# Optimization experiments

Hardware: AMD Instinct MI355X
Metric: run time of the kernel (lower is better)

## Reference

```python
import jax, jax.numpy as jnp
import numpy as np

NOT_EPSILON = 1.0
B, Q, K, T = 2, 512, 512, 256  # batch, num queries, num keys, dims


def swishmax(x, axis):
    # x * exp(x - max) / (sum(|x * exp(x - max)|) + 1)
    xexp = x * jnp.exp(x - jnp.max(x, axis=axis, keepdims=True))
    return xexp / (jnp.sum(jnp.abs(xexp), axis=axis, keepdims=True) + NOT_EPSILON)


def setup_inputs() -> dict:
    key = jax.random.key(0)
    ks = jax.random.split(key, 8)
    s = 1.0 / np.sqrt(T)
    return {
        "query_tokens": jax.random.normal(ks[0], (B, Q, T), jnp.float32),
        "key_tokens": jax.random.normal(ks[1], (B, K, T), jnp.float32),
        "value_tokens": jax.random.normal(ks[2], (B, K, T), jnp.float32),
        "Wk": jax.random.normal(ks[3], (T, T), jnp.float32) * s,
        "Wq": jax.random.normal(ks[4], (T, T), jnp.float32) * s,
        "Wva": jax.random.normal(ks[5], (T, T), jnp.float32) * s,
        "Wal": jax.random.normal(ks[6], (T, T), jnp.float32) * s,
        "Wvo": jax.random.normal(ks[7], (T, T), jnp.float32) * s,
    }


def reference(query_tokens, key_tokens, value_tokens, Wk, Wq, Wva, Wal, Wvo):
    # torch nn.Linear: y = x @ W.T (no biases)
    k = jnp.einsum('bkt,ut->bku', key_tokens, Wk)      # [B,K,T]
    q = jnp.einsum('bqt,ut->bqu', query_tokens, Wq)    # [B,Q,T]
    # elementwise outer product over token pairs: [B,K,Q,T]
    raw = k[:, :, None, :] * q[:, None, :, :]
    logits = jnp.einsum('bkqt,ut->bkqu', raw, Wal)     # [B,K,Q,T]
    scale = swishmax(logits, axis=-2)                  # normalize over Q
    v = jnp.einsum('bkt,ut->bku', value_tokens, Wva)   # [B,K,T]
    values_scaled = v[:, :, None, :] * scale           # [B,K,Q,T]
    value_sum = values_scaled.sum(axis=-3)             # sum over K -> [B,Q,T]
    return jnp.einsum('bqt,ut->bqu', value_sum, Wvo)   # [B,Q,T]
```

## Files before the change

### kernel.cpp

```cpp
#include <hip/hip_runtime.h>
#include <cstdint>


typedef short bf16x8 __attribute__((ext_vector_type(8)));
typedef float f32x4  __attribute__((ext_vector_type(4)));

__device__ inline float bf2f(short s) {
  return __uint_as_float(((unsigned)(unsigned short)s) << 16);
}
__device__ inline unsigned packrn(float lo, float hi) {
  return __builtin_amdgcn_perm(__float_as_uint(hi) + 0x8000u,
                               __float_as_uint(lo) + 0x8000u, 0x07060302u);
}
__device__ inline unsigned encM(float f) {
  unsigned k = (unsigned)__float_as_int(f);
  return (k & 0x80000000u) ? ~k : (k | 0x80000000u);
}
__device__ inline float decM(unsigned k) {
  int i = (k & 0x80000000u) ? (int)(k ^ 0x80000000u) : (int)~k;
  return __int_as_float(i);
}

#define FMA16()                                                                 \
  c[0][0] += a.x*w.x; c[0][1] += a.x*w.y; c[0][2] += a.x*w.z; c[0][3] += a.x*w.w; \
  c[1][0] += a.y*w.x; c[1][1] += a.y*w.y; c[1][2] += a.y*w.z; c[1][3] += a.y*w.w; \
  c[2][0] += a.z*w.x; c[2][1] += a.z*w.y; c[2][2] += a.z*w.z; c[2][3] += a.z*w.w; \
  c[3][0] += a.w*w.x; c[3][1] += a.w*w.y; c[3][2] += a.w*w.z; c[3][3] += a.w*w.w;

#define GEMM_BODY_RM(X, W)                                                      \
  __shared__ __align__(16) float As[16][68];                                    \
  __shared__ __align__(16) float Ws[16][68];                                    \
  const int tid = threadIdx.x;                                                  \
  const int tx4 = (tid & 15) * 4;                                               \
  const int ty4 = (tid >> 4) * 4;                                               \
  const int m0 = blockIdx.x * 64, u0 = blockIdx.y * 64;                         \
  const int lmi = tid >> 2, lc4 = (tid & 3) * 4;                                \
  float c[4][4] = {};                                                           \
  _Pragma("unroll 1")                                                           \
  for (int t0 = 0; t0 < 256; t0 += 16) {                                        \
    const float4 xa = *(const float4*)&(X)[(size_t)(m0 + lmi) * 256 + t0 + lc4];\
    const float4 wb = *(const float4*)&(W)[(size_t)(u0 + lmi) * 256 + t0 + lc4];\
    __syncthreads();                                                            \
    As[lc4 + 0][lmi] = xa.x; As[lc4 + 1][lmi] = xa.y;                           \
    As[lc4 + 2][lmi] = xa.z; As[lc4 + 3][lmi] = xa.w;                           \
    Ws[lc4 + 0][lmi] = wb.x; Ws[lc4 + 1][lmi] = wb.y;                           \
    Ws[lc4 + 2][lmi] = wb.z; Ws[lc4 + 3][lmi] = wb.w;                           \
    __syncthreads();                                                            \
    _Pragma("unroll")                                                           \
    for (int t = 0; t < 16; ++t) {                                              \
      const float4 a = *(const float4*)&As[t][ty4];                             \
      const float4 w = *(const float4*)&Ws[t][tx4];                             \
      FMA16();                                                                  \
    }                                                                           \
  }

__global__ __launch_bounds__(256) void proj3(
    const float* __restrict__ key, const float* __restrict__ value,
    const float* __restrict__ query, const float* __restrict__ Wk,
    const float* __restrict__ Wq, const float* __restrict__ Wva,
    const float* __restrict__ Wal, float* __restrict__ kproj,
    float* __restrict__ vproj, short* __restrict__ qpF,
    short* __restrict__ WalF, float* __restrict__ vsum)
{
  const int z = blockIdx.z;
  if (z == 3) {
    const int p = blockIdx.x * 4 + blockIdx.y;
    const int t256 = threadIdx.x;
#pragma unroll
    for (int e = 0; e < 4; ++e) {
      const int d = p * 1024 + t256 * 4 + e;
      const int j = d & 7, uu = (d >> 3) & 31, c8g = d >> 8;
      const int ucx = c8g >> 5, cc = c8g & 31;
      const float v = Wal[(ucx * 32 + uu) * 256 + cc * 8 + j];
      WalF[d] = (short)packrn(v, v);
    }
    float4* vz = (float4*)(vsum + p * 4096);
#pragma unroll
    for (int e = 0; e < 4; ++e) vz[t256 * 4 + e] = make_float4(0.f, 0.f, 0.f, 0.f);
    return;
  }
  const float* X = (z == 0) ? key : (z == 1) ? value : query;
  const float* W = (z == 0) ? Wk  : (z == 1) ? Wva   : Wq;
  GEMM_BODY_RM(X, W);
  if (z == 2) {
    const int tbase = u0 + tx4;
    const int ks = tbase >> 5, l4f = (tbase & 31) >> 3, j0 = tbase & 7;
#pragma unroll
    for (int i = 0; i < 4; ++i) {
      const int m = m0 + ty4 + i;
      const int bb = m >> 9, q = m & 511;
      const int g = q >> 4, l15q = q & 15;
      const size_t idx = ((size_t)(((bb * 32 + g) * 8 + ks) * 64) + l4f * 16 + l15q) * 8 + j0;
      uint2 s; s.x = packrn(c[i][0], c[i][1]); s.y = packrn(c[i][2], c[i][3]);
      *(uint2*)&qpF[idx] = s;
    }
  } else {
    float* C = (z == 0) ? kproj : vproj;
#pragma unroll
    for (int i = 0; i < 4; ++i)
      *(float4*)&C[(size_t)(m0 + ty4 + i) * 256 + u0 + tx4] =
          make_float4(c[i][0], c[i][1], c[i][2], c[i][3]);
  }
}

__global__ __launch_bounds__(256) void gemm_out(
    const float* __restrict__ X, const float* __restrict__ W, float* __restrict__ out)
{
  GEMM_BODY_RM(X, W);
#pragma unroll
  for (int i = 0; i < 4; ++i)
    *(float4*)&out[(size_t)(m0 + ty4 + i) * 256 + u0 + tx4] =
        make_float4(c[i][0], c[i][1], c[i][2], c[i][3]);
}

union Frag { bf16x8 v; unsigned u[4]; };

__global__ __launch_bounds__(512, 2) void kernelC(
    const short* __restrict__ qpF, const float* __restrict__ kproj,
    const float* __restrict__ vproj, const short* __restrict__ WalF,
    float* __restrict__ vsum)
{
  __shared__ __align__(16) short W2F[2][8192];
  __shared__ float vpS[32 * 33];
  __shared__ unsigned statM[96];
  __shared__ float statS[96];

  const int kt = blockIdx.x, uc = blockIdx.y, b = blockIdx.z;
  const int u0 = uc * 32, k0 = kt * 32;
  const int tid = threadIdx.x;
  const int lane = tid & 63, w = tid >> 6;
  const int l15 = lane & 15, l4 = lane >> 4;
  const int uu = tid & 31, c8 = tid >> 5;

  if (tid < 96) { statM[tid] = 0u; statS[tid] = 0.f; }
  {
    const int kk = tid >> 4, uu2 = (tid & 15) * 2;
    const float2 v2 = *(const float2*)&vproj[(size_t)(b * 512 + k0 + kk) * 256 + u0 + uu2];
    vpS[kk * 33 + uu2] = v2.x; vpS[kk * 33 + uu2 + 1] = v2.y;
  }

  float wl0[8], wl1[8];
  {
    const bf16x8 w0 = *(const bf16x8*)&WalF[((size_t)(uc * 32 + c8) * 32 + uu) * 8];
    const bf16x8 w1 = *(const bf16x8*)&WalF[((size_t)(uc * 32 + c8 + 16) * 32 + uu) * 8];
#pragma unroll
    for (int j = 0; j < 8; ++j) { wl0[j] = bf2f(w0[j]); wl1[j] = bf2f(w1[j]); }
  }

  const short* qbase = qpF + (size_t)b * 131072;
  Frag qa[4][8];
#pragma unroll
  for (int qg = 0; qg < 4; ++qg)
#pragma unroll
    for (int ks = 0; ks < 8; ++ks) {
      qa[qg][ks].v = *(const bf16x8*)&qbase[(((size_t)(w * 4 + qg) * 8 + ks) * 64 + lane) * 8];
      asm volatile("" : "+v"(qa[qg][ks].u[0]), "+v"(qa[qg][ks].u[1]),
                        "+v"(qa[qg][ks].u[2]), "+v"(qa[qg][ks].u[3]));
    }

  const int fb = (l4 * 32 + l15) * 8;
  const float* kq = &kproj[(long)(b * 512 + k0) * 256 + c8 * 8];

  {
    const f32x4 a0 = *(const f32x4*)(kq);
    const f32x4 a1 = *(const f32x4*)(kq + 4);
    const f32x4 b0 = *(const f32x4*)(kq + 128);
    const f32x4 b1 = *(const f32x4*)(kq + 132);
    uint4 st;
    st.x = packrn(wl0[0] * a0[0], wl0[1] * a0[1]);
    st.y = packrn(wl0[2] * a0[2], wl0[3] * a0[3]);
    st.z = packrn(wl0[4] * a1[0], wl0[5] * a1[1]);
    st.w = packrn(wl0[6] * a1[2], wl0[7] * a1[3]);
    *(uint4*)&W2F[0][(c8 * 32 + uu) * 8] = st;
    st.x = packrn(wl1[0] * b0[0], wl1[1] * b0[1]);
    st.y = packrn(wl1[2] * b0[2], wl1[3] * b0[3]);
    st.z = packrn(wl1[4] * b1[0], wl1[5] * b1[1]);
    st.w = packrn(wl1[6] * b1[2], wl1[7] * b1[3]);
    *(uint4*)&W2F[0][((c8 + 16) * 32 + uu) * 8] = st;
  }
  __syncthreads();

  const f32x4 z4 = {0.f, 0.f, 0.f, 0.f};
  f32x4 acc[4][2] = {z4, z4, z4, z4, z4, z4, z4, z4};

#pragma unroll 1
  for (int kk = 0; kk < 32; ++kk) {
    const int cs = kk & 1, ss = kk % 3;

    f32x4 a0, a1, b0, b1;
    if (kk < 31) {
      const float* kn = kq + (size_t)(kk + 1) * 256;
      a0 = *(const f32x4*)(kn);
      a1 = *(const f32x4*)(kn + 4);
      b0 = *(const f32x4*)(kn + 128);
      b1 = *(const f32x4*)(kn + 132);
    }

    f32x4 lg[4][2] = {z4, z4, z4, z4, z4, z4, z4, z4};
#pragma unroll
    for (int ks = 0; ks < 8; ++ks) {
      const bf16x8 f0 = *(const bf16x8*)&W2F[cs][fb + ks * 1024];
      const bf16x8 f1 = *(const bf16x8*)&W2F[cs][fb + ks * 1024 + 128];
#pragma unroll
      for (int qg = 0; qg < 4; ++qg) {
        lg[qg][0] = __builtin_amdgcn_mfma_f32_16x16x32_bf16(qa[qg][ks].v, f0, lg[qg][0], 0, 0, 0);
        lg[qg][1] = __builtin_amdgcn_mfma_f32_16x16x32_bf16(qa[qg][ks].v, f1, lg[qg][1], 0, 0, 0);
      }
    }
#pragma unroll
    for (int qg = 0; qg < 4; ++qg)
      asm volatile("" : "+v"(lg[qg][0]), "+v"(lg[qg][1]));

    if (kk < 31) {
      uint4 st;
      st.x = packrn(wl0[0] * a0[0], wl0[1] * a0[1]);
      st.y = packrn(wl0[2] * a0[2], wl0[3] * a0[3]);
      st.z = packrn(wl0[4] * a1[0], wl0[5] * a1[1]);
      st.w = packrn(wl0[6] * a1[2], wl0[7] * a1[3]);
      *(uint4*)&W2F[cs ^ 1][(c8 * 32 + uu) * 8] = st;
      st.x = packrn(wl1[0] * b0[0], wl1[1] * b0[1]);
      st.y = packrn(wl1[2] * b0[2], wl1[3] * b0[3]);
      st.z = packrn(wl1[4] * b1[0], wl1[5] * b1[1]);
      st.w = packrn(wl1[6] * b1[2], wl1[7] * b1[3]);
      *(uint4*)&W2F[cs ^ 1][((c8 + 16) * 32 + uu) * 8] = st;
    }

    float Mv[2], Sv[2];
#pragma unroll
    for (int ug = 0; ug < 2; ++ug) {
      const float m0q = fmaxf(fmaxf(lg[0][ug][0], lg[0][ug][1]), fmaxf(lg[0][ug][2], lg[0][ug][3]));
      const float m1q = fmaxf(fmaxf(lg[1][ug][0], lg[1][ug][1]), fmaxf(lg[1][ug][2], lg[1][ug][3]));
      const float m2q = fmaxf(fmaxf(lg[2][ug][0], lg[2][ug][1]), fmaxf(lg[2][ug][2], lg[2][ug][3]));
      const float m3q = fmaxf(fmaxf(lg[3][ug][0], lg[3][ug][1]), fmaxf(lg[3][ug][2], lg[3][ug][3]));
      float m = fmaxf(fmaxf(m0q, m1q), fmaxf(m2q, m3q));
      float sq[4];
#pragma unroll
      for (int qg = 0; qg < 4; ++qg) {
        float p0 = lg[qg][ug][0] * __expf(lg[qg][ug][0]);
        float p1 = lg[qg][ug][1] * __expf(lg[qg][ug][1]);
        float p2 = lg[qg][ug][2] * __expf(lg[qg][ug][2]);
        float p3 = lg[qg][ug][3] * __expf(lg[qg][ug][3]);
        lg[qg][ug][0] = p0; lg[qg][ug][1] = p1;
        lg[qg][ug][2] = p2; lg[qg][ug][3] = p3;
        sq[qg] = (fabsf(p0) + fabsf(p1)) + (fabsf(p2) + fabsf(p3));
      }
      float s = (sq[0] + sq[1]) + (sq[2] + sq[3]);
      m = fmaxf(m, __shfl_xor(m, 16));
      m = fmaxf(m, __shfl_xor(m, 32));
      s += __shfl_xor(s, 16);
      s += __shfl_xor(s, 32);
      Mv[ug] = m; Sv[ug] = s;
    }
    if (l4 == 0) {
      atomicMax(&statM[ss * 32 + l15],      encM(Mv[0]));
      atomicMax(&statM[ss * 32 + 16 + l15], encM(Mv[1]));
      atomicAdd(&statS[ss * 32 + l15],      Sv[0]);
      atomicAdd(&statS[ss * 32 + 16 + l15], Sv[1]);
    }
    __syncthreads();

#pragma unroll
    for (int ug = 0; ug < 2; ++ug) {
      const int ui = ug * 16 + l15;
      const float M = decM(statM[ss * 32 + ui]);
      const float S = statS[ss * 32 + ui];
      const float em = __expf(-M);
      const float g = vpS[kk * 33 + ui] * em * __builtin_amdgcn_rcpf(fmaf(S, em, 1.0f));
#pragma unroll
      for (int qg = 0; qg < 4; ++qg)
#pragma unroll
        for (int i = 0; i < 4; ++i)
          acc[qg][ug][i] = fmaf(g, lg[qg][ug][i], acc[qg][ug][i]);
    }
#pragma unroll
    for (int qg = 0; qg < 4; ++qg)
      asm volatile("" : "+v"(acc[qg][0]), "+v"(acc[qg][1]));

    const int rs = (kk + 2) % 3;
    if (tid < 32) { statM[rs * 32 + tid] = 0u; statS[rs * 32 + tid] = 0.f; }
  }

#pragma unroll
  for (int qg = 0; qg < 4; ++qg)
#pragma unroll
    for (int ug = 0; ug < 2; ++ug)
#pragma unroll
      for (int i = 0; i < 4; ++i)
        atomicAdd(&vsum[(size_t)(b * 512 + w * 64 + qg * 16 + l4 * 4 + i) * 256 +
                        u0 + ug * 16 + l15],
                  acc[qg][ug][i]);
}

extern "C" void kernel_launch(void* const* d_in, const int* in_sizes, int n_in,
                              void* d_out, int out_size, void* d_ws, size_t ws_size,
                              hipStream_t stream) {
  const float* query = (const float*)d_in[0];
  const float* key   = (const float*)d_in[1];
  const float* value = (const float*)d_in[2];
  const float* Wk    = (const float*)d_in[3];
  const float* Wq    = (const float*)d_in[4];
  const float* Wva   = (const float*)d_in[5];
  const float* Wal   = (const float*)d_in[6];
  const float* Wvo   = (const float*)d_in[7];
  float* ws = (float*)d_ws;

  float* kproj = ws;
  float* vproj = kproj + 262144;
  float* vsum  = vproj + 262144;
  short* qpF   = (short*)(vsum + 262144);
  short* WalF  = qpF + 262144;
  float* out   = (float*)d_out;

  proj3<<<dim3(16, 4, 4), 256, 0, stream>>>(key, value, query, Wk, Wq, Wva, Wal,
                                            kproj, vproj, qpF, WalF, vsum);
  kernelC<<<dim3(16, 8, 2), 512, 0, stream>>>(qpF, kproj, vproj, WalF, vsum);
  gemm_out<<<dim3(16, 4), 256, 0, stream>>>(vsum, Wvo, out);
}
```

Baseline: 192.3 us.

## Shrink GEMM tiles to 32 rows, prefetch next slab, split-K output GEMM

The shared FP32 GEMM body now uses 32x64 tiles instead of 64x64, which doubles the block count for the projection kernels and the output GEMM so more CUs are busy. The next K-slab is loaded from global memory while the current one is computed, a register prefetch. The output GEMM is split into two K halves that accumulate into the output with atomicAdd, so the proj3 kernel now also zeroes the output buffer. The costs are atomics and nondeterministic summation order, half of the A-loading threads idle, and extra zeroing work.

```diff
diff --git a/kernel.cpp b/kernel.cpp
--- a/kernel.cpp
+++ b/kernel.cpp
@@ -21,36 +21,39 @@
   return __int_as_float(i);
 }
 
-#define FMA16()                                                                 \
-  c[0][0] += a.x*w.x; c[0][1] += a.x*w.y; c[0][2] += a.x*w.z; c[0][3] += a.x*w.w; \
-  c[1][0] += a.y*w.x; c[1][1] += a.y*w.y; c[1][2] += a.y*w.z; c[1][3] += a.y*w.w; \
-  c[2][0] += a.z*w.x; c[2][1] += a.z*w.y; c[2][2] += a.z*w.z; c[2][3] += a.z*w.w; \
-  c[3][0] += a.w*w.x; c[3][1] += a.w*w.y; c[3][2] += a.w*w.z; c[3][3] += a.w*w.w;
-
-#define GEMM_BODY_RM(X, W)                                                      \
-  __shared__ __align__(16) float As[16][68];                                    \
+#define GEMM_BODY32(X, W, K0, K1)                                               \
+  __shared__ __align__(16) float As[16][36];                                    \
   __shared__ __align__(16) float Ws[16][68];                                    \
   const int tid = threadIdx.x;                                                  \
   const int tx4 = (tid & 15) * 4;                                               \
-  const int ty4 = (tid >> 4) * 4;                                               \
-  const int m0 = blockIdx.x * 64, u0 = blockIdx.y * 64;                         \
+  const int ty2 = (tid >> 4) * 2;                                               \
+  const int m0 = blockIdx.x * 32, u0 = blockIdx.y * 64;                         \
   const int lmi = tid >> 2, lc4 = (tid & 3) * 4;                                \
-  float c[4][4] = {};                                                           \
+  const bool hasA = tid < 128;                                                  \
+  float4 xa, wb;                                                                \
+  if (hasA) xa = *(const float4*)&(X)[(size_t)(m0 + lmi) * 256 + (K0) + lc4];   \
+  wb = *(const float4*)&(W)[(size_t)(u0 + lmi) * 256 + (K0) + lc4];             \
+  float c[2][4] = {};                                                           \
   _Pragma("unroll 1")                                                           \
-  for (int t0 = 0; t0 < 256; t0 += 16) {                                        \
-    const float4 xa = *(const float4*)&(X)[(size_t)(m0 + lmi) * 256 + t0 + lc4];\
-    const float4 wb = *(const float4*)&(W)[(size_t)(u0 + lmi) * 256 + t0 + lc4];\
+  for (int t0 = (K0); t0 < (K1); t0 += 16) {                                    \
     __syncthreads();                                                            \
-    As[lc4 + 0][lmi] = xa.x; As[lc4 + 1][lmi] = xa.y;                           \
-    As[lc4 + 2][lmi] = xa.z; As[lc4 + 3][lmi] = xa.w;                           \
+    if (hasA) {                                                                 \
+      As[lc4 + 0][lmi] = xa.x; As[lc4 + 1][lmi] = xa.y;                         \
+      As[lc4 + 2][lmi] = xa.z; As[lc4 + 3][lmi] = xa.w;                         \
+    }                                                                           \
     Ws[lc4 + 0][lmi] = wb.x; Ws[lc4 + 1][lmi] = wb.y;                           \
     Ws[lc4 + 2][lmi] = wb.z; Ws[lc4 + 3][lmi] = wb.w;                           \
     __syncthreads();                                                            \
+    if (t0 + 16 < (K1)) {                                                       \
+      if (hasA) xa = *(const float4*)&(X)[(size_t)(m0 + lmi) * 256 + t0 + 16 + lc4]; \
+      wb = *(const float4*)&(W)[(size_t)(u0 + lmi) * 256 + t0 + 16 + lc4];      \
+    }                                                                           \
     _Pragma("unroll")                                                           \
     for (int t = 0; t < 16; ++t) {                                              \
-      const float4 a = *(const float4*)&As[t][ty4];                             \
+      const float2 a = *(const float2*)&As[t][ty2];                             \
       const float4 w = *(const float4*)&Ws[t][tx4];                             \
-      FMA16();                                                                  \
+      c[0][0] += a.x*w.x; c[0][1] += a.x*w.y; c[0][2] += a.x*w.z; c[0][3] += a.x*w.w; \
+      c[1][0] += a.y*w.x; c[1][1] += a.y*w.y; c[1][2] += a.y*w.z; c[1][3] += a.y*w.w; \
     }                                                                           \
   }
 
@@ -60,11 +63,13 @@
     const float* __restrict__ Wq, const float* __restrict__ Wva,
     const float* __restrict__ Wal, float* __restrict__ kproj,
     float* __restrict__ vproj, short* __restrict__ qpF,
-    short* __restrict__ WalF, float* __restrict__ vsum)
+    short* __restrict__ WalF, float* __restrict__ vsum,
+    float* __restrict__ outz)
 {
   const int z = blockIdx.z;
   if (z == 3) {
     const int p = blockIdx.x * 4 + blockIdx.y;
+    if (p >= 64) return;
     const int t256 = threadIdx.x;
 #pragma unroll
     for (int e = 0; e < 4; ++e) {
@@ -75,19 +80,23 @@
       WalF[d] = (short)packrn(v, v);
     }
     float4* vz = (float4*)(vsum + p * 4096);
-#pragma unroll
-    for (int e = 0; e < 4; ++e) vz[t256 * 4 + e] = make_float4(0.f, 0.f, 0.f, 0.f);
+    float4* oz = (float4*)(outz + p * 4096);
+#pragma unroll
+    for (int e = 0; e < 4; ++e) {
+      vz[t256 * 4 + e] = make_float4(0.f, 0.f, 0.f, 0.f);
+      oz[t256 * 4 + e] = make_float4(0.f, 0.f, 0.f, 0.f);
+    }
     return;
   }
   const float* X = (z == 0) ? key : (z == 1) ? value : query;
   const float* W = (z == 0) ? Wk  : (z == 1) ? Wva   : Wq;
-  GEMM_BODY_RM(X, W);
+  GEMM_BODY32(X, W, 0, 256);
   if (z == 2) {
     const int tbase = u0 + tx4;
     const int ks = tbase >> 5, l4f = (tbase & 31) >> 3, j0 = tbase & 7;
 #pragma unroll
-    for (int i = 0; i < 4; ++i) {
-      const int m = m0 + ty4 + i;
+    for (int i = 0; i < 2; ++i) {
+      const int m = m0 + ty2 + i;
       const int bb = m >> 9, q = m & 511;
       const int g = q >> 4, l15q = q & 15;
       const size_t idx = ((size_t)(((bb * 32 + g) * 8 + ks) * 64) + l4f * 16 + l15q) * 8 + j0;
@@ -97,8 +106,8 @@
   } else {
     float* C = (z == 0) ? kproj : vproj;
 #pragma unroll
-    for (int i = 0; i < 4; ++i)
-      *(float4*)&C[(size_t)(m0 + ty4 + i) * 256 + u0 + tx4] =
+    for (int i = 0; i < 2; ++i)
+      *(float4*)&C[(size_t)(m0 + ty2 + i) * 256 + u0 + tx4] =
           make_float4(c[i][0], c[i][1], c[i][2], c[i][3]);
   }
 }
@@ -106,11 +115,13 @@
 __global__ __launch_bounds__(256) void gemm_out(
     const float* __restrict__ X, const float* __restrict__ W, float* __restrict__ out)
 {
-  GEMM_BODY_RM(X, W);
-#pragma unroll
-  for (int i = 0; i < 4; ++i)
-    *(float4*)&out[(size_t)(m0 + ty4 + i) * 256 + u0 + tx4] =
-        make_float4(c[i][0], c[i][1], c[i][2], c[i][3]);
+  const int kh = blockIdx.z * 128;
+  GEMM_BODY32(X, W, kh, kh + 128);
+#pragma unroll
+  for (int i = 0; i < 2; ++i)
+#pragma unroll
+    for (int j = 0; j < 4; ++j)
+      atomicAdd(&out[(size_t)(m0 + ty2 + i) * 256 + u0 + tx4 + j], c[i][j]);
 }
 
 union Frag { bf16x8 v; unsigned u[4]; };
@@ -311,8 +322,8 @@
   short* WalF  = qpF + 262144;
   float* out   = (float*)d_out;
 
-  proj3<<<dim3(16, 4, 4), 256, 0, stream>>>(key, value, query, Wk, Wq, Wva, Wal,
-                                            kproj, vproj, qpF, WalF, vsum);
+  proj3<<<dim3(32, 4, 4), 256, 0, stream>>>(key, value, query, Wk, Wq, Wva, Wal,
+                                            kproj, vproj, qpF, WalF, vsum, out);
   kernelC<<<dim3(16, 8, 2), 512, 0, stream>>>(qpF, kproj, vproj, WalF, vsum);
-  gemm_out<<<dim3(16, 4), 256, 0, stream>>>(vsum, Wvo, out);
-}
+  gemm_out<<<dim3(32, 4, 2), 256, 0, stream>>>(vsum, Wvo, out);
+}
```

New measurement: 191.9 us. About the same (-0.2%).
